# Kernel optimization log

Hardware: AMD Instinct MI355X
Metric: run time of the kernel (lower is better)

## Reference

```python
import jax, jax.numpy as jnp
import numpy as np

_OFF = 8
_M = 512  # coordinate hash base (> max coord + 2*_OFF)

def _enc(c):
    c64 = c.astype(np.int64) + _OFF
    return (c64[:, 0] * _M + c64[:, 1]) * _M + c64[:, 2]

def _kmap(out_c, in_c, scale):
    """Per-offset neighbor map: maps[k, j] = index into in_c of voxel out_c[j] + scale*offset_k, or -1."""
    ik = _enc(in_c)
    order = np.argsort(ik)
    sk = ik[order]
    maps = np.full((27, len(out_c)), -1, np.int32)
    k = 0
    for dx in (-1, 0, 1):
        for dy in (-1, 0, 1):
            for dz in (-1, 0, 1):
                ck = _enc(out_c + np.array([dx, dy, dz]) * scale)
                pos = np.clip(np.searchsorted(sk, ck), 0, len(sk) - 1)
                hit = sk[pos] == ck
                maps[k] = np.where(hit, order[pos].astype(np.int32), -1)
                k += 1
    return maps


def setup_inputs() -> dict:
    rng = np.random.default_rng(0)
    c = rng.integers(0, 160, size=(300000, 3))
    c0 = np.unique(c, axis=0)[:200000]          # stride-1 voxels
    c2 = np.unique((c0 // 2) * 2, axis=0)       # stride-2 voxels
    c4 = np.unique((c2 // 4) * 4, axis=0)       # stride-4 voxels

    maps = {
        'map0':  jnp.asarray(_kmap(c0, c0, 1)),   # block0  (s=1)
        'map1':  jnp.asarray(_kmap(c2, c0, 1)),   # block1  (s=2 down)
        'map2':  jnp.asarray(_kmap(c4, c2, 2)),   # block2  (s=2 down)
        'map2t': jnp.asarray(_kmap(c2, c4, 2)),   # block2_tr (transposed)
        'map1t': jnp.asarray(_kmap(c0, c2, 1)),   # block1_tr (transposed)
        'map0t': jnp.asarray(_kmap(c0, c0, 1)),   # block0_tr (s=1)
    }

    key = jax.random.key(0)
    ks = jax.random.split(key, 8)

    def w(k, cin, cout):
        return jax.random.normal(k, (27, cin, cout), jnp.float32) / np.sqrt(27.0 * cin)

    nf, e = 16, 32
    inp = {'feats': jax.random.normal(ks[0], (c0.shape[0], nf), jnp.float32)}
    inp['W0'] = w(ks[1], nf, e);          inp['g0'] = jnp.ones((e,));        inp['b0'] = jnp.zeros((e,))
    inp['W1'] = w(ks[2], e, 2 * e);       inp['g1'] = jnp.ones((2 * e,));    inp['b1'] = jnp.zeros((2 * e,))
    inp['W2'] = w(ks[3], 2 * e, 4 * e);   inp['g2'] = jnp.ones((4 * e,));    inp['b2'] = jnp.zeros((4 * e,))
    inp['W2t'] = w(ks[4], 4 * e, 2 * e);  inp['g2t'] = jnp.ones((2 * e,));   inp['b2t'] = jnp.zeros((2 * e,))
    inp['W1t'] = w(ks[5], 4 * e, 2 * e);  inp['g1t'] = jnp.ones((2 * e,));   inp['b1t'] = jnp.zeros((2 * e,))
    inp['W0t'] = w(ks[6], 3 * e, 2)
    inp.update(maps)
    return inp


def _sconv(x, W, m):
    """Sparse 3D conv as gather-GEMM-scatter. x:[Nin,Cin], W:[27,Cin,Cout], m:[27,Nout]."""
    valid = m >= 0
    idx = jnp.maximum(m, 0)
    acc0 = jnp.zeros((m.shape[1], W.shape[2]), x.dtype)

    def body(acc, kw):
        mk, vk, Wk = kw
        g = jnp.where(vk[:, None], x[mk], 0.0)
        return acc + g @ Wk, None

    out, _ = jax.lax.scan(body, acc0, (idx, valid, W))
    return out


def _bn_relu(x, g, b, eps=1e-5):
    mu = x.mean(0)
    var = x.var(0)
    return jax.nn.relu((x - mu) * jax.lax.rsqrt(var + eps) * g + b)


def reference(feats, W0, g0, b0, W1, g1, b1, W2, g2, b2,
              W2t, g2t, b2t, W1t, g1t, b1t, W0t,
              map0, map1, map2, map2t, map1t, map0t):
    s1 = _bn_relu(_sconv(feats, W0, map0), g0, b0)   # [N0, 32]
    s2 = _bn_relu(_sconv(s1, W1, map1), g1, b1)      # [N1, 64]
    s4 = _bn_relu(_sconv(s2, W2, map2), g2, b2)      # [N2, 128]
    d2 = _bn_relu(_sconv(s4, W2t, map2t), g2t, b2t)  # [N1, 64]
    d2 = jnp.concatenate([d2, s2], axis=1)           # [N1, 128] skip cat
    d1 = _bn_relu(_sconv(d2, W1t, map1t), g1t, b1t)  # [N0, 64]
    d1 = jnp.concatenate([d1, s1], axis=1)           # [N0, 96] skip cat
    return _sconv(d1, W0t, map0t)                    # [N0, 2]
```

## Files before the change

kernel.cpp:

```cpp
#include <hip/hip_runtime.h>
#include <cstddef>
#include <cstdint>

#define BN_EPS 1e-5f

typedef float f4 __attribute__((ext_vector_type(4)));
typedef float f32x4 __attribute__((ext_vector_type(4)));
typedef _Float16 h2 __attribute__((ext_vector_type(2)));
typedef _Float16 h8 __attribute__((ext_vector_type(8)));

#if defined(__has_builtin)
#if __has_builtin(__builtin_amdgcn_fdot2)
#define DOT2(a, b, c) __builtin_amdgcn_fdot2((a), (b), (c), false)
#endif
#endif
#ifndef DOT2
#define DOT2(a, b, c) fmaf((float)(a)[1], (float)(b)[1], fmaf((float)(a)[0], (float)(b)[0], (c)))
#endif

template<int CIN, int COUT>
__global__ __launch_bounds__(256)
void wtrans_h(const float* __restrict__ W, _Float16* __restrict__ Wh)
{
    const int t = blockIdx.x * 256 + threadIdx.x;
    constexpr int TOTAL = 27 * (CIN / 8) * COUT;
    if (t >= TOTAL) return;
    const int co = t % COUT;
    const int rest = t / COUT;
    const int t8 = rest % (CIN / 8);
    const int k  = rest / (CIN / 8);
    h8 v;
    #pragma unroll
    for (int u = 0; u < 8; ++u)
        v[u] = (_Float16)W[((size_t)k * CIN + t8 * 8 + u) * COUT + co];
    *(h8*)(Wh + (size_t)t * 8) = v;
}

template<int CIN, int COUT>
__global__ __launch_bounds__(256)
void wtrans_mf(const float* __restrict__ W, _Float16* __restrict__ Wm)
{
    constexpr int NT = CIN / 32;
    constexpr int NC = COUT / 16;
    const int t = blockIdx.x * 256 + threadIdx.x;
    constexpr int TOTAL = 27 * NT * NC * 64;
    if (t >= TOTAL) return;
    const int lane = t & 63;
    int rest = t >> 6;
    const int ct = rest % NC; rest /= NC;
    const int tt = rest % NT;
    const int k  = rest / NT;
    const int cin0 = tt * 32 + (lane >> 4) * 8;
    const int co   = ct * 16 + (lane & 15);
    h8 v;
    #pragma unroll
    for (int u = 0; u < 8; ++u)
        v[u] = (_Float16)W[((size_t)k * CIN + cin0 + u) * COUT + co];
    *(h8*)(Wm + (size_t)t * 8) = v;
}

__global__ __launch_bounds__(256)
void wtrans_mf0(const float* __restrict__ W, _Float16* __restrict__ Wm0)
{
    const int t = blockIdx.x * 256 + threadIdx.x;
    constexpr int TOTAL = 27 * 2 * 32;
    if (t >= TOTAL) return;
    const int co = t % 32;
    const int s  = (t / 32) % 2;
    const int k  = t / 64;
    h8 v;
    #pragma unroll
    for (int u = 0; u < 8; ++u)
        v[u] = (_Float16)W[((size_t)k * 16 + s * 8 + u) * 32 + co];
    *(h8*)(Wm0 + (size_t)t * 8) = v;
}

__global__ __launch_bounds__(256)
void map_transpose(const int* __restrict__ map, int Nout,
                   int* __restrict__ mapT)
{
    __shared__ int s[256][28];
    const int tid  = threadIdx.x;
    const int base = blockIdx.x * 256;
    const int j    = base + tid;
    for (int k = 0; k < 27; ++k)
        s[tid][k] = (j < Nout) ? map[(size_t)k * Nout + j] : -1;
    __syncthreads();
    for (int i = tid; i < 256 * 32; i += 256) {
        const int r = i >> 5, c = i & 31;
        if (base + r < Nout)
            mapT[(size_t)(base + r) * 32 + c] = (c < 27) ? s[r][c] : -1;
    }
}

__global__ __launch_bounds__(256)
void map_transpose_grp(const int* __restrict__ map, int Nout, int Npad,
                       int* __restrict__ mapT, int* __restrict__ gcursor,
                       int* __restrict__ order)
{
    __shared__ int s[256][28];
    __shared__ int hist[9], basec[9], cur[9];
    const int tid  = threadIdx.x;
    const int base = blockIdx.x * 256;
    const int j    = base + tid;
    if (tid < 9) { hist[tid] = 0; cur[tid] = 0; }
    for (int k = 0; k < 27; ++k)
        s[tid][k] = (j < Nout) ? map[(size_t)k * Nout + j] : -1;
    __syncthreads();
    for (int i = tid; i < 256 * 32; i += 256) {
        const int r = i >> 5, c = i & 31;
        if (base + r < Nout)
            mapT[(size_t)(base + r) * 32 + c] = (c < 27) ? s[r][c] : -1;
    }
    int c9 = 8;
    if (j < Nout) {
        #pragma unroll 1
        for (int k = 0; k < 27; ++k) {
            if (s[tid][k] >= 0) {
                const int dz = k % 3, dy = (k / 3) % 3, dx = k / 9;
                c9 = ((dx != 1) << 2) | ((dy != 1) << 1) | (int)(dz != 1);
                break;
            }
        }
        atomicAdd(&hist[c9], 1);
    }
    __syncthreads();
    if (tid < 9 && hist[tid] > 0)
        basec[tid] = atomicAdd(&gcursor[tid], hist[tid]);
    __syncthreads();
    if (j < Nout) {
        const int lpos = atomicAdd(&cur[c9], 1);
        order[(size_t)c9 * Npad + basec[c9] + lpos] = j;
    }
}

template<int CIN, int CINA, int COUT>
__global__ __launch_bounds__(256)
void sconv_r1(const _Float16* __restrict__ xA, const _Float16* __restrict__ xB,
              const _Float16* __restrict__ Wh, const int* __restrict__ mapT,
              int Nout, _Float16* __restrict__ out)
{
    constexpr int CINB = CIN - CINA;
    constexpr int CPL  = COUT / 64;
    constexpr int NT   = CIN / 8;
    const int lane = threadIdx.x & 63;
    const int j    = blockIdx.x * 4 + (threadIdx.x >> 6);

    int mk = -1;
    if (j < Nout && lane < 32) mk = mapT[(size_t)j * 32 + lane];
    unsigned long long act = __ballot(mk >= 0);

    float acc[CPL];
    #pragma unroll
    for (int c = 0; c < CPL; ++c) acc[c] = 0.f;

    while (act) {
        const int k = (int)__builtin_ctzll(act);
        act &= act - 1;
        const int m = __builtin_amdgcn_readlane(mk, k);

        const _Float16* pA = xA + (size_t)m * CINA;
        const _Float16* pB = nullptr;
        if constexpr (CINB > 0) pB = xB + (size_t)m * CINB;

        const _Float16* Wk = Wh + (size_t)k * NT * COUT * 8;

        #pragma unroll
        for (int t = 0; t < NT; ++t) {
            const int ci = t * 8;
            h8 wv[CPL];
            #pragma unroll
            for (int c = 0; c < CPL; ++c)
                wv[c] = *(const h8*)(Wk + ((size_t)t * COUT + c * 64 + lane) * 8);
            const _Float16* p;
            if constexpr (CINB > 0)
                p = (ci < CINA) ? (pA + ci) : (pB + (ci - CINA));
            else
                p = pA + ci;
            const h8 xv = *(const h8*)p;
            const h2* xp = (const h2*)&xv;
            #pragma unroll
            for (int q = 0; q < 4; ++q) {
                #pragma unroll
                for (int c = 0; c < CPL; ++c) {
                    const h2* wp = (const h2*)&wv[c];
                    acc[c] = DOT2(xp[q], wp[q], acc[c]);
                }
            }
        }
    }

    if (j < Nout) {
        #pragma unroll
        for (int c = 0; c < CPL; ++c)
            out[(size_t)j * COUT + c * 64 + lane] = (_Float16)acc[c];
    }
}

__global__ __launch_bounds__(256)
void sconv_mf0(const float* __restrict__ x, const _Float16* __restrict__ Wm0,
               const int* __restrict__ map, int Nout,
               _Float16* __restrict__ out, const float* __restrict__ zrow)
{
    const int lane = threadIdx.x & 63;
    const int wave = threadIdx.x >> 6;
    const int row0 = (blockIdx.x * 4 + wave) * 16;

    __shared__ int smap[4][16][28];

    int mk[16];
    bool anyv = false;
    #pragma unroll
    for (int r = 0; r < 16; ++r) {
        const int j = row0 + r;
        mk[r] = (lane < 27 && j < Nout) ? map[(size_t)lane * Nout + j] : -1;
        anyv |= (mk[r] >= 0);
    }
    unsigned long long act = __ballot(anyv);

    if (lane < 27) {
        #pragma unroll
        for (int r = 0; r < 16; ++r)
            smap[wave][r][lane] = mk[r];
    }

    f32x4 accH[2], accL[2];
    #pragma unroll
    for (int c = 0; c < 2; ++c) {
        accH[c] = (f32x4){0.f, 0.f, 0.f, 0.f};
        accL[c] = (f32x4){0.f, 0.f, 0.f, 0.f};
    }

    const int rrow = lane & 15;
    const int kseg = lane >> 4;
    const int half = kseg & 1;
    const bool useK1 = (kseg < 2);

    while (act) {
        const int k1 = (int)__builtin_ctzll(act);
        act &= act - 1;
        int k2 = -1;
        if (act) {
            k2 = (int)__builtin_ctzll(act);
            act &= act - 1;
        }
        const int ks = useK1 ? k1 : k2;
        int m = -1;
        if (ks >= 0) m = smap[wave][rrow][ks];

        const float* px = (m >= 0) ? (x + (size_t)m * 16 + half * 8)
                                   : (zrow + half * 8);
        const f4 x0 = *(const f4*)px;
        const f4 x1 = *(const f4*)(px + 4);
        h8 aH, aL;
        #pragma unroll
        for (int u = 0; u < 4; ++u) {
            const float v0 = x0[u], v1 = x1[u];
            const _Float16 h0 = (_Float16)v0;
            const _Float16 h1 = (_Float16)v1;
            aH[u]     = h0;
            aH[u + 4] = h1;
            aL[u]     = (_Float16)((v0 - (float)h0) * 2048.f);
            aL[u + 4] = (_Float16)((v1 - (float)h1) * 2048.f);
        }

        const int ksafe = (ks >= 0) ? ks : 0;
        const _Float16* wb = Wm0 + ((size_t)(ksafe * 2 + half) * 32) * 8;
        #pragma unroll
        for (int c = 0; c < 2; ++c) {
            const h8 b = *(const h8*)(wb + (size_t)(c * 16 + rrow) * 8);
            accH[c] = __builtin_amdgcn_mfma_f32_16x16x32_f16(aH, b, accH[c], 0, 0, 0);
            accL[c] = __builtin_amdgcn_mfma_f32_16x16x32_f16(aL, b, accL[c], 0, 0, 0);
        }
    }

    #pragma unroll
    for (int c = 0; c < 2; ++c) {
        #pragma unroll
        for (int r = 0; r < 4; ++r) {
            const int j = row0 + kseg * 4 + r;
            if (j < Nout)
                out[(size_t)j * 32 + c * 16 + rrow] =
                    (_Float16)(accH[c][r] + accL[c][r] * (1.f / 2048.f));
        }
    }
}

template<int CIN, int CINA, int COUT>
__global__ __launch_bounds__(256)
void sconv_mf(const _Float16* __restrict__ xA, const _Float16* __restrict__ xB,
              const _Float16* __restrict__ Wm, const int* __restrict__ map,
              int Nout, _Float16* __restrict__ out,
              const _Float16* __restrict__ zrh)
{
    constexpr int CINB = CIN - CINA;
    constexpr int NT = CIN / 32;
    constexpr int NC = COUT / 16;
    static_assert(CINA % 32 == 0, "CINA must be a multiple of 32");
    const int lane = threadIdx.x & 63;
    const int wave = threadIdx.x >> 6;
    const int row0 = (blockIdx.x * 4 + wave) * 32;

    __shared__ int smap[4][32][28];

    bool anyv = false;
    #pragma unroll
    for (int r = 0; r < 32; ++r) {
        const int j = row0 + r;
        const int v = (lane < 27 && j < Nout) ? map[(size_t)lane * Nout + j] : -1;
        if (lane < 27) smap[wave][r][lane] = v;
        anyv |= (v >= 0);
    }
    unsigned long long act = __ballot(anyv) & 0x7FFFFFFull;

    f32x4 acc[2][NC];
    #pragma unroll
    for (int tt = 0; tt < 2; ++tt)
        #pragma unroll
        for (int c = 0; c < NC; ++c) acc[tt][c] = (f32x4){0.f, 0.f, 0.f, 0.f};

    const int rrow = lane & 15;
    const int kseg = lane >> 4;

    auto loada = [&](int k, h8 a[2][NT]) {
        #pragma unroll
        for (int tt = 0; tt < 2; ++tt) {
            const int m = smap[wave][tt * 16 + rrow][k];
            #pragma unroll
            for (int t = 0; t < NT; ++t) {
                const int cin0 = t * 32 + kseg * 8;
                const _Float16* pa;
                if (m >= 0) {
                    if (CINB > 0 && t * 32 >= CINA)
                        pa = xB + (size_t)m * CINB + (cin0 - CINA);
                    else
                        pa = xA + (size_t)m * CINA + cin0;
                } else {
                    pa = zrh;
                }
                a[tt][t] = *(const h8*)pa;
            }
        }
    };
    auto compute = [&](int k, h8 a[2][NT]) {
        const _Float16* Wk = Wm + ((size_t)k * NT * NC * 64 + lane) * 8;
        #pragma unroll
        for (int t = 0; t < NT; ++t) {
            #pragma unroll
            for (int c = 0; c < NC; ++c) {
                const h8 b = *(const h8*)(Wk + (size_t)(t * NC + c) * 64 * 8);
                acc[0][c] = __builtin_amdgcn_mfma_f32_16x16x32_f16(a[0][t], b, acc[0][c], 0, 0, 0);
                acc[1][c] = __builtin_amdgcn_mfma_f32_16x16x32_f16(a[1][t], b, acc[1][c], 0, 0, 0);
            }
        }
    };

    h8 aC[2][NT], aN[2][NT];
    int kC = -1;
    if (act) {
        kC = (int)__builtin_ctzll(act);
        act &= act - 1;
        loada(kC, aC);
    }
    while (kC >= 0) {
        int kN = -1;
        if (act) {
            kN = (int)__builtin_ctzll(act);
            act &= act - 1;
            loada(kN, aN);
        }
        compute(kC, aC);
        #pragma unroll
        for (int tt = 0; tt < 2; ++tt)
            #pragma unroll
            for (int t = 0; t < NT; ++t) aC[tt][t] = aN[tt][t];
        kC = kN;
    }

    #pragma unroll
    for (int tt = 0; tt < 2; ++tt) {
        #pragma unroll
        for (int c = 0; c < NC; ++c) {
            #pragma unroll
            for (int r = 0; r < 4; ++r) {
                const int j = row0 + tt * 16 + kseg * 4 + r;
                if (j < Nout)
                    out[(size_t)j * COUT + c * 16 + rrow] = (_Float16)acc[tt][c][r];
            }
        }
    }
}

template<int CIN, int CINA, int COUT>
__global__ __launch_bounds__(256)
void sconv_mf_g(const _Float16* __restrict__ xA, const _Float16* __restrict__ xB,
                const _Float16* __restrict__ Wm, const int* __restrict__ mapT,
                const int* __restrict__ order, int NTOT, int Nout,
                _Float16* __restrict__ out, const _Float16* __restrict__ zrh)
{
    constexpr int CINB = CIN - CINA;
    constexpr int NT = CIN / 32;
    constexpr int NC = COUT / 16;
    static_assert(CINA % 32 == 0, "CINA must be a multiple of 32");
    const int lane = threadIdx.x & 63;
    const int wave = threadIdx.x >> 6;
    const int wrow0 = (blockIdx.x * 4 + wave) * 32;

    __shared__ int sjr[4][32];
    __shared__ int smap[4][32][28];

    int jreg = -1;
    if (lane < 32) {
        const int idx = wrow0 + lane;
        if (idx < NTOT) jreg = order[idx];
    }
    if (!__ballot(jreg >= 0)) return;
    if (lane < 32) sjr[wave][lane] = jreg;

    bool anyv = false;
    #pragma unroll
    for (int r = 0; r < 32; ++r) {
        const int jr = sjr[wave][r];
        int v = -1;
        if (jr >= 0 && lane < 27) v = mapT[(size_t)jr * 32 + lane];
        if (lane < 27) smap[wave][r][lane] = v;
        anyv |= (v >= 0);
    }
    unsigned long long act = __ballot(anyv) & 0x7FFFFFFull;

    f32x4 acc[2][NC];
    #pragma unroll
    for (int tt = 0; tt < 2; ++tt)
        #pragma unroll
        for (int c = 0; c < NC; ++c) acc[tt][c] = (f32x4){0.f, 0.f, 0.f, 0.f};

    const int rrow = lane & 15;
    const int kseg = lane >> 4;

    auto loada = [&](int k, h8 a[2][NT]) {
        #pragma unroll
        for (int tt = 0; tt < 2; ++tt) {
            const int m = smap[wave][tt * 16 + rrow][k];
            #pragma unroll
            for (int t = 0; t < NT; ++t) {
                const int cin0 = t * 32 + kseg * 8;
                const _Float16* pa;
                if (m >= 0) {
                    if (CINB > 0 && t * 32 >= CINA)
                        pa = xB + (size_t)m * CINB + (cin0 - CINA);
                    else
                        pa = xA + (size_t)m * CINA + cin0;
                } else {
                    pa = zrh;
                }
                a[tt][t] = *(const h8*)pa;
            }
        }
    };
    auto compute = [&](int k, h8 a[2][NT]) {
        const _Float16* Wk = Wm + ((size_t)k * NT * NC * 64 + lane) * 8;
        #pragma unroll
        for (int t = 0; t < NT; ++t) {
            #pragma unroll
            for (int c = 0; c < NC; ++c) {
                const h8 b = *(const h8*)(Wk + (size_t)(t * NC + c) * 64 * 8);
                acc[0][c] = __builtin_amdgcn_mfma_f32_16x16x32_f16(a[0][t], b, acc[0][c], 0, 0, 0);
                acc[1][c] = __builtin_amdgcn_mfma_f32_16x16x32_f16(a[1][t], b, acc[1][c], 0, 0, 0);
            }
        }
    };

    h8 aC[2][NT], aN[2][NT];
    int kC = -1;
    if (act) {
        kC = (int)__builtin_ctzll(act);
        act &= act - 1;
        loada(kC, aC);
    }
    while (kC >= 0) {
        int kN = -1;
        if (act) {
            kN = (int)__builtin_ctzll(act);
            act &= act - 1;
            loada(kN, aN);
        }
        compute(kC, aC);
        #pragma unroll
        for (int tt = 0; tt < 2; ++tt)
            #pragma unroll
            for (int t = 0; t < NT; ++t) aC[tt][t] = aN[tt][t];
        kC = kN;
    }

    #pragma unroll
    for (int tt = 0; tt < 2; ++tt) {
        #pragma unroll
        for (int c = 0; c < NC; ++c) {
            #pragma unroll
            for (int r = 0; r < 4; ++r) {
                const int j = sjr[wave][tt * 16 + kseg * 4 + r];
                if (j >= 0)
                    out[(size_t)j * COUT + c * 16 + rrow] = (_Float16)acc[tt][c][r];
            }
        }
    }
}

__global__ __launch_bounds__(256)
void sconv0t(const _Float16* __restrict__ d1, const _Float16* __restrict__ s1,
             const float* __restrict__ W ,
             const int* __restrict__ map, int N, float* __restrict__ out,
             const _Float16* __restrict__ zrh)
{
    const int tid  = threadIdx.x;
    const int lane = tid & 63;
    const int l32  = tid & 31;
    const int j    = blockIdx.x * 8 + (tid >> 5);

    int mk = (l32 < 27 && j < N) ? map[(size_t)l32 * N + j] : -1;
    const unsigned long long bal = __ballot(mk >= 0);
    unsigned int act = (unsigned int)((bal | (bal >> 32)) & 0x7FFFFFFu);

    float a0 = 0.f, a1 = 0.f;
    while (act) {
        const int k = (int)__builtin_ctz(act);
        act &= act - 1;
        const int m = __shfl(mk, (lane & 32) + k);
        const _Float16* p1 = (m >= 0) ? (d1 + (size_t)m * 64) : zrh;
        const _Float16* p2 = (m >= 0) ? (s1 + (size_t)m * 32) : zrh;
        const float* w = W + (size_t)k * 96 * 2;
        const float x0 = (float)p1[l32];
        const float x1 = (float)p1[l32 + 32];
        const float x2 = (float)p2[l32];
        a0 = fmaf(x0, w[l32 * 2 + 0], a0);
        a1 = fmaf(x0, w[l32 * 2 + 1], a1);
        a0 = fmaf(x1, w[(l32 + 32) * 2 + 0], a0);
        a1 = fmaf(x1, w[(l32 + 32) * 2 + 1], a1);
        a0 = fmaf(x2, w[(l32 + 64) * 2 + 0], a0);
        a1 = fmaf(x2, w[(l32 + 64) * 2 + 1], a1);
    }
    #pragma unroll
    for (int off = 1; off < 32; off <<= 1) {
        a0 += __shfl_xor(a0, off, 32);
        a1 += __shfl_xor(a1, off, 32);
    }
    if (l32 == 0 && j < N) {
        out[(size_t)j * 2 + 0] = a0;
        out[(size_t)j * 2 + 1] = a1;
    }
}

template<int C>
__global__ __launch_bounds__(256)
void bn_reduce_v(const _Float16* __restrict__ x, int N,
                 float* __restrict__ sums)
{
    constexpr int CV = C / 8;
    const int tid  = threadIdx.x;
    const int lane = tid & 63;
    const int wave = tid >> 6;
    const size_t total  = (size_t)N * CV;
    const size_t stride = (size_t)gridDim.x * 256;
    const size_t gid    = (size_t)blockIdx.x * 256 + tid;

    float s[8], s2[8];
    #pragma unroll
    for (int u = 0; u < 8; ++u) { s[u] = 0.f; s2[u] = 0.f; }

    for (size_t v = gid; v < total; v += stride) {
        const h8 hv = *(const h8*)(x + v * 8);
        #pragma unroll
        for (int u = 0; u < 8; ++u) {
            const float f = (float)hv[u];
            s[u] += f;
            s2[u] += f * f;
        }
    }

    #pragma unroll
    for (int off = CV; off < 64; off <<= 1) {
        #pragma unroll
        for (int u = 0; u < 8; ++u) {
            s[u]  += __shfl_xor(s[u], off);
            s2[u] += __shfl_xor(s2[u], off);
        }
    }

    __shared__ float shs[4][16][8];
    __shared__ float shq[4][16][8];
    if (lane < CV) {
        #pragma unroll
        for (int u = 0; u < 8; ++u) {
            shs[wave][lane][u] = s[u];
            shq[wave][lane][u] = s2[u];
        }
    }
    __syncthreads();
    if (tid < C) {
        const int ph = tid >> 3, u = tid & 7;
        float ts = 0.f, tq = 0.f;
        #pragma unroll
        for (int w = 0; w < 4; ++w) {
            ts += shs[w][ph][u];
            tq += shq[w][ph][u];
        }
        atomicAdd(&sums[tid], ts);
        atomicAdd(&sums[C + tid], tq);
    }
}

template<int C>
__global__ __launch_bounds__(256)
void bn_apply_v(_Float16* __restrict__ x, int N,
                const float* __restrict__ sums,
                const float* __restrict__ g, const float* __restrict__ b)
{
    constexpr int CV = C / 8;
    const size_t total  = (size_t)N * CV;
    const size_t stride = (size_t)gridDim.x * 256;
    const size_t gid    = (size_t)blockIdx.x * 256 + threadIdx.x;
    const int phase = (int)(gid % CV);

    const float invN = 1.0f / (float)N;
    float sc[8], sh[8];
    #pragma unroll
    for (int u = 0; u < 8; ++u) {
        const int c = phase * 8 + u;
        const float mean = sums[c] * invN;
        float var = sums[C + c] * invN - mean * mean;
        var = fmaxf(var, 0.f);
        sc[u] = g[c] * rsqrtf(var + BN_EPS);
        sh[u] = b[c] - mean * sc[u];
    }

    for (size_t v = gid; v < total; v += stride) {
        h8 hv = *(h8*)(x + v * 8);
        #pragma unroll
        for (int u = 0; u < 8; ++u) {
            const float f = fmaf((float)hv[u], sc[u], sh[u]);
            hv[u] = (_Float16)(f > 0.f ? f : 0.f);
        }
        *(h8*)(x + v * 8) = hv;
    }
}

extern "C" void kernel_launch(void* const* d_in, const int* in_sizes, int n_in,
                              void* d_out, int out_size, void* d_ws, size_t ws_size,
                              hipStream_t stream)
{
    const float* feats = (const float*)d_in[0];
    const float* W0  = (const float*)d_in[1];
    const float* g0  = (const float*)d_in[2];
    const float* b0  = (const float*)d_in[3];
    const float* W1  = (const float*)d_in[4];
    const float* g1  = (const float*)d_in[5];
    const float* b1  = (const float*)d_in[6];
    const float* W2  = (const float*)d_in[7];
    const float* g2  = (const float*)d_in[8];
    const float* b2  = (const float*)d_in[9];
    const float* W2t = (const float*)d_in[10];
    const float* g2t = (const float*)d_in[11];
    const float* b2t = (const float*)d_in[12];
    const float* W1t = (const float*)d_in[13];
    const float* g1t = (const float*)d_in[14];
    const float* b1t = (const float*)d_in[15];
    const float* W0t = (const float*)d_in[16];
    const int* map0  = (const int*)d_in[17];
    const int* map1  = (const int*)d_in[18];
    const int* map2  = (const int*)d_in[19];
    const int* map2t = (const int*)d_in[20];
    const int* map1t = (const int*)d_in[21];
    const int* map0t = (const int*)d_in[22];

    const int N0 = in_sizes[0] / 16;
    const int N1 = in_sizes[18] / 27;
    const int N2 = in_sizes[19] / 27;

    const int Npad0 = (N0 + 15) & ~15;
    const int Npad1 = (N1 + 15) & ~15;

    float* ws = (float*)d_ws;
    float* sums  = ws;
    float* sums0 = sums;
    float* sums1 = sums + 64;
    float* sums2 = sums + 192;
    float* sums3 = sums + 448;
    float* sums4 = sums + 576;
    float* zrow  = sums + 704;
    int*   gcnt  = (int*)(zrow + 128);
    _Float16* Wm0h = (_Float16*)(gcnt + 64);
    _Float16* Wh1  = Wm0h + 27 * 2 * 32 * 8;
    _Float16* Wh2  = Wh1 + 27 * 32 * 64;
    _Float16* Wh2t = Wh2 + 27 * 64 * 128;
    _Float16* Wh1t = Wh2t + 27 * 128 * 64;
    _Float16* y0 = Wh1t + 27 * 128 * 64;
    _Float16* y1 = y0 + (size_t)N0 * 32;
    _Float16* y2 = y1 + (size_t)N1 * 64;
    _Float16* y3 = y2 + (size_t)N2 * 128;
    _Float16* y4 = y3 + (size_t)N1 * 64;
    int* mapT = (int*)(y4 + (size_t)N0 * 64);
    int* orderA = mapT + (size_t)N0 * 32;
    int* orderB = orderA + (size_t)9 * Npad1;
    const _Float16* zrh = (const _Float16*)zrow;

    (void)hipMemsetAsync(sums, 0, (704 + 128 + 64) * sizeof(float), stream);
    (void)hipMemsetAsync(orderA, 0xFF,
                         (size_t)9 * (Npad1 + Npad0) * sizeof(int), stream);

    wtrans_mf0<<<(27 * 2 * 32 + 255) / 256, 256, 0, stream>>>(W0, Wm0h);
    wtrans_h<32, 64><<<(27 * 4 * 64 + 255) / 256, 256, 0, stream>>>(W1, Wh1);
    wtrans_mf<64, 128><<<(27 * 2 * 8 * 64 + 255) / 256, 256, 0, stream>>>(W2, Wh2);
    wtrans_mf<128, 64><<<(27 * 4 * 4 * 64 + 255) / 256, 256, 0, stream>>>(W2t, Wh2t);
    wtrans_mf<128, 64><<<(27 * 4 * 4 * 64 + 255) / 256, 256, 0, stream>>>(W1t, Wh1t);

    sconv_mf0<<<(N0 + 63) / 64, 256, 0, stream>>>(
        feats, Wm0h, map0, N0, y0, zrow);
    bn_reduce_v<32><<<512, 256, 0, stream>>>(y0, N0, sums0);
    bn_apply_v<32><<<1024, 256, 0, stream>>>(y0, N0, sums0, g0, b0);

    map_transpose<<<(N1 + 255) / 256, 256, 0, stream>>>(map1, N1, mapT);
    sconv_r1<32, 32, 64><<<(N1 + 3) / 4, 256, 0, stream>>>(
        y0, nullptr, Wh1, mapT, N1, y1);
    bn_reduce_v<64><<<512, 256, 0, stream>>>(y1, N1, sums1);
    bn_apply_v<64><<<1024, 256, 0, stream>>>(y1, N1, sums1, g1, b1);

    sconv_mf<64, 64, 128><<<(N2 + 127) / 128, 256, 0, stream>>>(
        y1, nullptr, Wh2, map2, N2, y2, zrh);
    bn_reduce_v<128><<<512, 256, 0, stream>>>(y2, N2, sums2);
    bn_apply_v<128><<<1024, 256, 0, stream>>>(y2, N2, sums2, g2, b2);

    map_transpose_grp<<<(N1 + 255) / 256, 256, 0, stream>>>(
        map2t, N1, Npad1, mapT, gcnt, orderA);
    sconv_mf_g<128, 128, 64><<<(9 * Npad1 + 127) / 128, 256, 0, stream>>>(
        y2, nullptr, Wh2t, mapT, orderA, 9 * Npad1, N1, y3, zrh);
    bn_reduce_v<64><<<512, 256, 0, stream>>>(y3, N1, sums3);
    bn_apply_v<64><<<1024, 256, 0, stream>>>(y3, N1, sums3, g2t, b2t);

    map_transpose_grp<<<(N0 + 255) / 256, 256, 0, stream>>>(
        map1t, N0, Npad0, mapT, gcnt + 32, orderB);
    sconv_mf_g<128, 64, 64><<<(9 * Npad0 + 127) / 128, 256, 0, stream>>>(
        y3, y1, Wh1t, mapT, orderB, 9 * Npad0, N0, y4, zrh);
    bn_reduce_v<64><<<512, 256, 0, stream>>>(y4, N0, sums4);
    bn_apply_v<64><<<1024, 256, 0, stream>>>(y4, N0, sums4, g1t, b1t);

    sconv0t<<<(N0 + 7) / 8, 256, 0, stream>>>(y4, y0, W0t, map0t, N0,
                                              (float*)d_out, zrh);
}
```

Before: 692.8 us.

## Run block1 conv on MFMA kernel and pair offsets in final conv loop

Replaces the dot2-based sconv_r1 path for the stride-2 down conv (with its map transpose) by the existing MFMA sconv_mf kernel, using the MFMA weight layout for W1. It also unrolls the final 96->2 conv loop to handle two active offsets per iteration, with vectorized half2 feature loads and float4/float2 weight loads. The goal is to raise matrix throughput, drop an extra transpose pass, and add memory-level parallelism in the last layer. The cost is more registers in the final kernel, and MFMA tiling of 32-channel inputs may be less efficient.

```diff
diff --git a/kernel.cpp b/kernel.cpp
--- a/kernel.cpp
+++ b/kernel.cpp
@@ -4,37 +4,11 @@
 
 #define BN_EPS 1e-5f
 
+typedef float f2 __attribute__((ext_vector_type(2)));
 typedef float f4 __attribute__((ext_vector_type(4)));
 typedef float f32x4 __attribute__((ext_vector_type(4)));
 typedef _Float16 h2 __attribute__((ext_vector_type(2)));
 typedef _Float16 h8 __attribute__((ext_vector_type(8)));
-
-#if defined(__has_builtin)
-#if __has_builtin(__builtin_amdgcn_fdot2)
-#define DOT2(a, b, c) __builtin_amdgcn_fdot2((a), (b), (c), false)
-#endif
-#endif
-#ifndef DOT2
-#define DOT2(a, b, c) fmaf((float)(a)[1], (float)(b)[1], fmaf((float)(a)[0], (float)(b)[0], (c)))
-#endif
-
-template<int CIN, int COUT>
-__global__ __launch_bounds__(256)
-void wtrans_h(const float* __restrict__ W, _Float16* __restrict__ Wh)
-{
-    const int t = blockIdx.x * 256 + threadIdx.x;
-    constexpr int TOTAL = 27 * (CIN / 8) * COUT;
-    if (t >= TOTAL) return;
-    const int co = t % COUT;
-    const int rest = t / COUT;
-    const int t8 = rest % (CIN / 8);
-    const int k  = rest / (CIN / 8);
-    h8 v;
-    #pragma unroll
-    for (int u = 0; u < 8; ++u)
-        v[u] = (_Float16)W[((size_t)k * CIN + t8 * 8 + u) * COUT + co];
-    *(h8*)(Wh + (size_t)t * 8) = v;
-}
 
 template<int CIN, int COUT>
 __global__ __launch_bounds__(256)
@@ -76,24 +50,6 @@
 }
 
 __global__ __launch_bounds__(256)
-void map_transpose(const int* __restrict__ map, int Nout,
-                   int* __restrict__ mapT)
-{
-    __shared__ int s[256][28];
-    const int tid  = threadIdx.x;
-    const int base = blockIdx.x * 256;
-    const int j    = base + tid;
-    for (int k = 0; k < 27; ++k)
-        s[tid][k] = (j < Nout) ? map[(size_t)k * Nout + j] : -1;
-    __syncthreads();
-    for (int i = tid; i < 256 * 32; i += 256) {
-        const int r = i >> 5, c = i & 31;
-        if (base + r < Nout)
-            mapT[(size_t)(base + r) * 32 + c] = (c < 27) ? s[r][c] : -1;
-    }
-}
-
-__global__ __launch_bounds__(256)
 void map_transpose_grp(const int* __restrict__ map, int Nout, int Npad,
                        int* __restrict__ mapT, int* __restrict__ gcursor,
                        int* __restrict__ order)
@@ -134,69 +90,6 @@
     }
 }
 
-template<int CIN, int CINA, int COUT>
-__global__ __launch_bounds__(256)
-void sconv_r1(const _Float16* __restrict__ xA, const _Float16* __restrict__ xB,
-              const _Float16* __restrict__ Wh, const int* __restrict__ mapT,
-              int Nout, _Float16* __restrict__ out)
-{
-    constexpr int CINB = CIN - CINA;
-    constexpr int CPL  = COUT / 64;
-    constexpr int NT   = CIN / 8;
-    const int lane = threadIdx.x & 63;
-    const int j    = blockIdx.x * 4 + (threadIdx.x >> 6);
-
-    int mk = -1;
-    if (j < Nout && lane < 32) mk = mapT[(size_t)j * 32 + lane];
-    unsigned long long act = __ballot(mk >= 0);
-
-    float acc[CPL];
-    #pragma unroll
-    for (int c = 0; c < CPL; ++c) acc[c] = 0.f;
-
-    while (act) {
-        const int k = (int)__builtin_ctzll(act);
-        act &= act - 1;
-        const int m = __builtin_amdgcn_readlane(mk, k);
-
-        const _Float16* pA = xA + (size_t)m * CINA;
-        const _Float16* pB = nullptr;
-        if constexpr (CINB > 0) pB = xB + (size_t)m * CINB;
-
-        const _Float16* Wk = Wh + (size_t)k * NT * COUT * 8;
-
-        #pragma unroll
-        for (int t = 0; t < NT; ++t) {
-            const int ci = t * 8;
-            h8 wv[CPL];
-            #pragma unroll
-            for (int c = 0; c < CPL; ++c)
-                wv[c] = *(const h8*)(Wk + ((size_t)t * COUT + c * 64 + lane) * 8);
-            const _Float16* p;
-            if constexpr (CINB > 0)
-                p = (ci < CINA) ? (pA + ci) : (pB + (ci - CINA));
-            else
-                p = pA + ci;
-            const h8 xv = *(const h8*)p;
-            const h2* xp = (const h2*)&xv;
-            #pragma unroll
-            for (int q = 0; q < 4; ++q) {
-                #pragma unroll
-                for (int c = 0; c < CPL; ++c) {
-                    const h2* wp = (const h2*)&wv[c];
-                    acc[c] = DOT2(xp[q], wp[q], acc[c]);
-                }
-            }
-        }
-    }
-
-    if (j < Nout) {
-        #pragma unroll
-        for (int c = 0; c < CPL; ++c)
-            out[(size_t)j * COUT + c * 64 + lane] = (_Float16)acc[c];
-    }
-}
-
 __global__ __launch_bounds__(256)
 void sconv_mf0(const float* __restrict__ x, const _Float16* __restrict__ Wm0,
                const int* __restrict__ map, int Nout,
@@ -523,21 +416,43 @@
 
     float a0 = 0.f, a1 = 0.f;
     while (act) {
-        const int k = (int)__builtin_ctz(act);
+        const int k1 = (int)__builtin_ctz(act);
         act &= act - 1;
-        const int m = __shfl(mk, (lane & 32) + k);
-        const _Float16* p1 = (m >= 0) ? (d1 + (size_t)m * 64) : zrh;
-        const _Float16* p2 = (m >= 0) ? (s1 + (size_t)m * 32) : zrh;
-        const float* w = W + (size_t)k * 96 * 2;
-        const float x0 = (float)p1[l32];
-        const float x1 = (float)p1[l32 + 32];
-        const float x2 = (float)p2[l32];
-        a0 = fmaf(x0, w[l32 * 2 + 0], a0);
-        a1 = fmaf(x0, w[l32 * 2 + 1], a1);
-        a0 = fmaf(x1, w[(l32 + 32) * 2 + 0], a0);
-        a1 = fmaf(x1, w[(l32 + 32) * 2 + 1], a1);
-        a0 = fmaf(x2, w[(l32 + 64) * 2 + 0], a0);
-        a1 = fmaf(x2, w[(l32 + 64) * 2 + 1], a1);
+        int k2 = -1;
+        if (act) { k2 = (int)__builtin_ctz(act); act &= act - 1; }
+        const int k2s = (k2 >= 0) ? k2 : k1;
+
+        const int m1 = __shfl(mk, (lane & 32) + k1);
+        int m2 = __shfl(mk, (lane & 32) + k2s);
+        if (k2 < 0) m2 = -1;
+
+        const _Float16* p1a = (m1 >= 0) ? (d1 + (size_t)m1 * 64) : zrh;
+        const _Float16* p1b = (m1 >= 0) ? (s1 + (size_t)m1 * 32) : zrh;
+        const _Float16* p2a = (m2 >= 0) ? (d1 + (size_t)m2 * 64) : zrh;
+        const _Float16* p2b = (m2 >= 0) ? (s1 + (size_t)m2 * 32) : zrh;
+        const h2 xa1 = *(const h2*)(p1a + 2 * l32);
+        const float xs1 = (float)p1b[l32];
+        const h2 xa2 = *(const h2*)(p2a + 2 * l32);
+        const float xs2 = (float)p2b[l32];
+
+        const f4 wa1 = *(const f4*)(W + (size_t)k1 * 192 + 4 * l32);
+        const f2 ws1 = *(const f2*)(W + (size_t)k1 * 192 + 128 + 2 * l32);
+        const f4 wa2 = *(const f4*)(W + (size_t)k2s * 192 + 4 * l32);
+        const f2 ws2 = *(const f2*)(W + (size_t)k2s * 192 + 128 + 2 * l32);
+
+        a0 = fmaf((float)xa1[0], wa1[0], a0);
+        a1 = fmaf((float)xa1[0], wa1[1], a1);
+        a0 = fmaf((float)xa1[1], wa1[2], a0);
+        a1 = fmaf((float)xa1[1], wa1[3], a1);
+        a0 = fmaf(xs1, ws1[0], a0);
+        a1 = fmaf(xs1, ws1[1], a1);
+
+        a0 = fmaf((float)xa2[0], wa2[0], a0);
+        a1 = fmaf((float)xa2[0], wa2[1], a1);
+        a0 = fmaf((float)xa2[1], wa2[2], a0);
+        a1 = fmaf((float)xa2[1], wa2[3], a1);
+        a0 = fmaf(xs2, ws2[0], a0);
+        a1 = fmaf(xs2, ws2[1], a1);
     }
     #pragma unroll
     for (int off = 1; off < 32; off <<= 1) {
@@ -708,7 +623,7 @@
                          (size_t)9 * (Npad1 + Npad0) * sizeof(int), stream);
 
     wtrans_mf0<<<(27 * 2 * 32 + 255) / 256, 256, 0, stream>>>(W0, Wm0h);
-    wtrans_h<32, 64><<<(27 * 4 * 64 + 255) / 256, 256, 0, stream>>>(W1, Wh1);
+    wtrans_mf<32, 64><<<(27 * 1 * 4 * 64 + 255) / 256, 256, 0, stream>>>(W1, Wh1);
     wtrans_mf<64, 128><<<(27 * 2 * 8 * 64 + 255) / 256, 256, 0, stream>>>(W2, Wh2);
     wtrans_mf<128, 64><<<(27 * 4 * 4 * 64 + 255) / 256, 256, 0, stream>>>(W2t, Wh2t);
     wtrans_mf<128, 64><<<(27 * 4 * 4 * 64 + 255) / 256, 256, 0, stream>>>(W1t, Wh1t);
@@ -718,9 +633,8 @@
     bn_reduce_v<32><<<512, 256, 0, stream>>>(y0, N0, sums0);
     bn_apply_v<32><<<1024, 256, 0, stream>>>(y0, N0, sums0, g0, b0);
 
-    map_transpose<<<(N1 + 255) / 256, 256, 0, stream>>>(map1, N1, mapT);
-    sconv_r1<32, 32, 64><<<(N1 + 3) / 4, 256, 0, stream>>>(
-        y0, nullptr, Wh1, mapT, N1, y1);
+    sconv_mf<32, 32, 64><<<(N1 + 127) / 128, 256, 0, stream>>>(
+        y0, nullptr, Wh1, map1, N1, y1, zrh);
     bn_reduce_v<64><<<512, 256, 0, stream>>>(y1, N1, sums1);
     bn_apply_v<64><<<1024, 256, 0, stream>>>(y1, N1, sums1, g1, b1);
 
```

New measurement: 662.9 us. 4.3% less time.
